# Kernel tuning notes

Hardware: AMD Instinct MI355X
Metric: run time of the kernel (lower is better)

## Reference

```python
import jax, jax.numpy as jnp
import numpy as np

B, S, H = 16, 4096, 512   # batch, seq frames, conv_dim[-1]
G, V, D = 2, 320, 256     # groups, codevectors per group, codevector_dim


def setup_inputs() -> dict:
    key = jax.random.key(0)
    k1, k2, k3 = jax.random.split(key, 3)
    hidden_states = jax.random.normal(k1, (B, S, H), dtype=jnp.float32)
    W = jax.random.normal(k2, (H, G * V), dtype=jnp.float32) * 0.02
    b = jnp.zeros((G * V,), dtype=jnp.float32)
    codevectors = jax.random.normal(k3, (1, G * V, D // G), dtype=jnp.float32)
    return {"hidden_states": hidden_states, "W": W, "b": b,
            "codevectors": codevectors, "num_groups": G}


def reference(hidden_states, W, b, codevectors, num_groups):
    Bb, Ss, Hh = hidden_states.shape
    GV = W.shape[1]
    g = num_groups
    v = GV // g
    d = codevectors.shape[-1]
    BT = Bb * Ss

    # weight_proj: [B,S,H] @ [H, G*V] -> logits per (token, group, var)
    logits = (hidden_states @ W + b).reshape(BT, g, v)

    # eval path: hard argmax one-hot over codevectors per group
    idx = jnp.argmax(logits, axis=-1)              # [BT, g] int

    # one-hot x codebook multiply-reduce == gather from codebook
    cb = codevectors.reshape(g, v, d)              # [g, v, d]
    gathered = cb[jnp.arange(g)[None, :], idx]     # [BT, g, d]
    out = gathered.reshape(Bb, Ss, g * d)          # [B, S, codevector_dim]

    # perplexity over one-hot probs: marginal = mean of one-hots = counts/BT
    marginal = jnp.zeros((g, v), dtype=jnp.float32)
    marginal = marginal.at[jnp.arange(g)[None, :], idx].add(1.0) / BT
    perplexity = jnp.exp(-jnp.sum(marginal * jnp.log(marginal + 1e-7), axis=-1)).sum()

    return out, perplexity
```

## Files before the change

kernel.cpp:

```cpp
#include <hip/hip_runtime.h>
#include <hip/hip_bf16.h>
#include <hip/hip_fp8.h>

constexpr int BT = 65536;
constexpr int K  = 512;
constexpr int V  = 320;
constexpr int G  = 2;
constexpr int Dg = 128;
constexpr int MT = 64;
constexpr int NSTEP = 8;
constexpr size_t WS_IMG = 4096;

using f32x4 = __attribute__((ext_vector_type(4))) float;

static __device__ __forceinline__ unsigned cvt4(float a, float b, float c, float d) {
#if __has_builtin(__builtin_amdgcn_cvt_pk_fp8_f32)
    int r = 0;
    r = __builtin_amdgcn_cvt_pk_fp8_f32(a, b, r, false);
    r = __builtin_amdgcn_cvt_pk_fp8_f32(c, d, r, true);
    return (unsigned)r;
#else
    __hip_fp8_e4m3 ha(a), hb(b), hc(c), hd(d);
    return (unsigned)ha.__x | ((unsigned)hb.__x << 8) |
           ((unsigned)hc.__x << 16) | ((unsigned)hd.__x << 24);
#endif
}
static __device__ __forceinline__ long long mk64(unsigned lo, unsigned hi) {
    return (long long)(((unsigned long long)hi << 32) | lo);
}
static __device__ __forceinline__ f32x4 mfma_fp8(long long a, long long b, f32x4 c) {
    return __builtin_amdgcn_mfma_f32_16x16x32_fp8_fp8(a, b, c, 0, 0, 0);
}

__global__ __launch_bounds__(256) void vq_prep(const float* __restrict__ Wm,
                                               unsigned char* __restrict__ img)
{
    int id   = blockIdx.x * 256 + threadIdx.x;
    int lane = id & 63;
    int r    = id >> 6;
    int nt   = r % 5;  r /= 5;
    int wc   = r & 3;  r >>= 2;
    int s    = r & 7;
    int g    = r >> 3;
    int col  = g * V + wc * 80 + nt * 16 + (lane & 15);
    int kb   = s * 64 + (lane >> 4) * 8;
    float v0[8], v1[8];
#pragma unroll
    for (int j = 0; j < 8; ++j) {
        v0[j] = 16.0f * Wm[(size_t)(kb + j) * 640 + col];
        v1[j] = 16.0f * Wm[(size_t)(kb + 32 + j) * 640 + col];
    }
    *reinterpret_cast<uint4*>(img + (size_t)id * 16) =
        make_uint4(cvt4(v0[0], v0[1], v0[2], v0[3]), cvt4(v0[4], v0[5], v0[6], v0[7]),
                   cvt4(v1[0], v1[1], v1[2], v1[3]), cvt4(v1[4], v1[5], v1[6], v1[7]));
}

__global__ __launch_bounds__(512) void vq_main(
    const float* __restrict__ hs, const unsigned char* __restrict__ img,
    const float* __restrict__ bv, const float* __restrict__ cbv,
    float* __restrict__ out, unsigned int* __restrict__ hist)
{
    __shared__ __align__(16) unsigned char smem[8192];

    const int tid  = threadIdx.x;
    const int bid  = blockIdx.x;
    const int g    = (bid >> 3) & 1;
    const int rblk = (bid & 7) | ((bid >> 4) << 3);
    const int r0   = rblk * MT;
    const int w    = tid >> 6;
    const int lane = tid & 63;
    const int l4   = lane & 15;
    const int wc   = w & 3;
    const int h    = w >> 2;

    f32x4 acc[2][5] = {};

    const int arow = tid >> 3, akq = tid & 7;
    const float* aptr = hs + (size_t)(r0 + arow) * K + akq * 8;
    const int awoff = (arow >> 4) * 1024 + ((arow & 15) + 16 * (akq & 3)) * 16 + (akq >> 2) * 8;
    const int a_rd0 = (h * 2 + 0) * 1024 + lane * 16;
    const int a_rd1 = (h * 2 + 1) * 1024 + lane * 16;
    const unsigned char* bwv = img + (size_t)g * 163840 + wc * 5120 + (size_t)lane * 16;

    auto packA = [&](float4 x, float4 y, int sel) {
        *reinterpret_cast<uint2*>(&smem[sel * 4096 + awoff]) =
            make_uint2(cvt4(x.x, x.y, x.z, x.w), cvt4(y.x, y.y, y.z, y.w));
    };

    float4 aX[2], aY[2];
    aX[0] = *reinterpret_cast<const float4*>(aptr);
    aY[0] = *reinterpret_cast<const float4*>(aptr + 4);
    packA(aX[0], aY[0], 0);
    aX[1] = *reinterpret_cast<const float4*>(aptr + 64);
    aY[1] = *reinterpret_cast<const float4*>(aptr + 64 + 4);
    __syncthreads();

#pragma unroll
    for (int s = 0; s < NSTEP; ++s) {
        const int cur = s & 1, nxt = cur ^ 1;
        if (s + 1 < NSTEP) packA(aX[nxt], aY[nxt], nxt);
        if (s + 2 < NSTEP) {
            aX[cur] = *reinterpret_cast<const float4*>(aptr + (s + 2) * 64);
            aY[cur] = *reinterpret_cast<const float4*>(aptr + (s + 2) * 64 + 4);
        }
        const unsigned char* bs = bwv + (size_t)s * 20480;
        __builtin_amdgcn_s_setprio(1);
        {
            uint4 b0 = *reinterpret_cast<const uint4*>(bs);
            uint4 b1 = *reinterpret_cast<const uint4*>(bs + 1024);
            uint4 b2 = *reinterpret_cast<const uint4*>(bs + 2048);
            uint4 b3 = *reinterpret_cast<const uint4*>(bs + 3072);
            uint4 b4 = *reinterpret_cast<const uint4*>(bs + 4096);
            uint4 a0 = *reinterpret_cast<const uint4*>(&smem[cur * 4096 + a_rd0]);
            uint4 a1 = *reinterpret_cast<const uint4*>(&smem[cur * 4096 + a_rd1]);
            long long a0k0 = mk64(a0.x, a0.y), a0k1 = mk64(a0.z, a0.w);
            long long a1k0 = mk64(a1.x, a1.y), a1k1 = mk64(a1.z, a1.w);
            uint4 bb[5] = {b0, b1, b2, b3, b4};
#pragma unroll
            for (int nt = 0; nt < 5; ++nt) {
                long long bk0 = mk64(bb[nt].x, bb[nt].y), bk1 = mk64(bb[nt].z, bb[nt].w);
                acc[0][nt] = mfma_fp8(a0k0, bk0, acc[0][nt]);
                acc[0][nt] = mfma_fp8(a0k1, bk1, acc[0][nt]);
                acc[1][nt] = mfma_fp8(a1k0, bk0, acc[1][nt]);
                acc[1][nt] = mfma_fp8(a1k1, bk1, acc[1][nt]);
            }
        }
        __builtin_amdgcn_s_setprio(0);
        __syncthreads();
    }

    float biasv[5];
#pragma unroll
    for (int nt = 0; nt < 5; ++nt) biasv[nt] = 16.0f * bv[g * V + wc * 80 + nt * 16 + l4];

    float* red_v = reinterpret_cast<float*>(smem);
    int*   red_i = reinterpret_cast<int*>(smem + 1024);
    int*   idx_s = reinterpret_cast<int*>(smem + 2048);

#pragma unroll
    for (int mt = 0; mt < 2; ++mt) {
#pragma unroll
        for (int reg = 0; reg < 4; ++reg) {
            float bestv = acc[mt][0][reg] + biasv[0];
            int   besti = wc * 80 + l4;
#pragma unroll
            for (int nt = 1; nt < 5; ++nt) {
                float v = acc[mt][nt][reg] + biasv[nt];
                int   ci = wc * 80 + nt * 16 + l4;
                if (v > bestv) { bestv = v; besti = ci; }
            }
#pragma unroll
            for (int m = 1; m < 16; m <<= 1) {
                float ov = __shfl_xor(bestv, m);
                int   oi = __shfl_xor(besti, m);
                if (ov > bestv || (ov == bestv && oi < besti)) { bestv = ov; besti = oi; }
            }
            if (l4 == 0) {
                int row = h * 32 + mt * 16 + (lane >> 4) * 4 + reg;
                red_v[row * 4 + wc] = bestv;
                red_i[row * 4 + wc] = besti;
            }
        }
    }
    __syncthreads();

    int my_bi = -1;
    if (tid < MT) {
        float bb = red_v[tid * 4]; int bi = red_i[tid * 4];
#pragma unroll
        for (int c = 1; c < 4; ++c) {
            float v = red_v[tid * 4 + c]; int ii = red_i[tid * 4 + c];
            if (v > bb || (v == bb && ii < bi)) { bb = v; bi = ii; }
        }
        idx_s[tid] = bi;
        my_bi = bi;
    }
    __syncthreads();

#pragma unroll
    for (int i = 0; i < 4; ++i) {
        int idx = i * 512 + tid;
        int row = idx >> 5;
        int d4  = idx & 31;
        int vi  = idx_s[row];
        float4 val = *reinterpret_cast<const float4*>(&cbv[((size_t)(g * V + vi)) * Dg + d4 * 4]);
        *reinterpret_cast<float4*>(&out[((size_t)(r0 + row)) * (G * Dg) + g * Dg + d4 * 4]) = val;
    }
    if (my_bi >= 0) atomicAdd(&hist[g * V + my_bi], 1u);
}

__global__ void vq_ppl(const unsigned int* __restrict__ hist, float* __restrict__ outp)
{
    int lane = threadIdx.x;
    float ppl = 0.0f;
    for (int g = 0; g < G; ++g) {
        float local = 0.0f;
        for (int v = lane; v < V; v += 64) {
            float m = (float)hist[g * V + v] * (1.0f / (float)BT);
            local += m * logf(m + 1e-7f);
        }
#pragma unroll
        for (int off = 32; off; off >>= 1) local += __shfl_down(local, off);
        if (lane == 0) ppl += expf(-local);
    }
    if (lane == 0) outp[0] = ppl;
}

extern "C" void kernel_launch(void* const* d_in, const int* in_sizes, int n_in,
                              void* d_out, int out_size, void* d_ws, size_t ws_size,
                              hipStream_t stream)
{
    const float* hs  = (const float*)d_in[0];
    const float* Wm  = (const float*)d_in[1];
    const float* bv  = (const float*)d_in[2];
    const float* cbv = (const float*)d_in[3];
    float* out = (float*)d_out;

    unsigned int*  hist = (unsigned int*)d_ws;
    unsigned char* img  = (unsigned char*)d_ws + WS_IMG;

    hipMemsetAsync(d_ws, 0, G * V * sizeof(unsigned int), stream);
    vq_prep<<<80, 256, 0, stream>>>(Wm, img);
    vq_main<<<2048, 512, 0, stream>>>(hs, img, bv, cbv, out, hist);
    vq_ppl<<<1, 64, 0, stream>>>(hist, out + (size_t)BT * G * Dg);
}
```

Measured before the change: 88.60 us.

## Process both groups per block, staging full fp8 A tile in LDS once

New measurement: 98.87 us. 1.12x slower.

```diff
diff --git a/kernel.cpp b/kernel.cpp
--- a/kernel.cpp
+++ b/kernel.cpp
@@ -60,62 +60,56 @@
     const float* __restrict__ bv, const float* __restrict__ cbv,
     float* __restrict__ out, unsigned int* __restrict__ hist)
 {
-    __shared__ __align__(16) unsigned char smem[8192];
+    __shared__ __align__(16) unsigned char smem[35072];
 
     const int tid  = threadIdx.x;
     const int bid  = blockIdx.x;
-    const int g    = (bid >> 3) & 1;
-    const int rblk = (bid & 7) | ((bid >> 4) << 3);
-    const int r0   = rblk * MT;
+    const int r0   = bid * MT;
     const int w    = tid >> 6;
     const int lane = tid & 63;
     const int l4   = lane & 15;
     const int wc   = w & 3;
     const int h    = w >> 2;
 
-    f32x4 acc[2][5] = {};
-
-    const int arow = tid >> 3, akq = tid & 7;
-    const float* aptr = hs + (size_t)(r0 + arow) * K + akq * 8;
-    const int awoff = (arow >> 4) * 1024 + ((arow & 15) + 16 * (akq & 3)) * 16 + (akq >> 2) * 8;
+    {
+        const int arow = tid >> 3, akq = tid & 7;
+        const float* aptr = hs + (size_t)(r0 + arow) * K + akq * 8;
+        const int awoff = (arow >> 4) * 1024 + ((arow & 15) + 16 * (akq & 3)) * 16 + (akq >> 2) * 8;
+#pragma unroll
+        for (int s = 0; s < NSTEP; ++s) {
+            float4 x = *reinterpret_cast<const float4*>(aptr + s * 64);
+            float4 y = *reinterpret_cast<const float4*>(aptr + s * 64 + 4);
+            *reinterpret_cast<uint2*>(&smem[s * 4096 + awoff]) =
+                make_uint2(cvt4(x.x, x.y, x.z, x.w), cvt4(y.x, y.y, y.z, y.w));
+        }
+    }
+    __syncthreads();
+
     const int a_rd0 = (h * 2 + 0) * 1024 + lane * 16;
     const int a_rd1 = (h * 2 + 1) * 1024 + lane * 16;
-    const unsigned char* bwv = img + (size_t)g * 163840 + wc * 5120 + (size_t)lane * 16;
-
-    auto packA = [&](float4 x, float4 y, int sel) {
-        *reinterpret_cast<uint2*>(&smem[sel * 4096 + awoff]) =
-            make_uint2(cvt4(x.x, x.y, x.z, x.w), cvt4(y.x, y.y, y.z, y.w));
-    };
-
-    float4 aX[2], aY[2];
-    aX[0] = *reinterpret_cast<const float4*>(aptr);
-    aY[0] = *reinterpret_cast<const float4*>(aptr + 4);
-    packA(aX[0], aY[0], 0);
-    aX[1] = *reinterpret_cast<const float4*>(aptr + 64);
-    aY[1] = *reinterpret_cast<const float4*>(aptr + 64 + 4);
-    __syncthreads();
-
-#pragma unroll
-    for (int s = 0; s < NSTEP; ++s) {
-        const int cur = s & 1, nxt = cur ^ 1;
-        if (s + 1 < NSTEP) packA(aX[nxt], aY[nxt], nxt);
-        if (s + 2 < NSTEP) {
-            aX[cur] = *reinterpret_cast<const float4*>(aptr + (s + 2) * 64);
-            aY[cur] = *reinterpret_cast<const float4*>(aptr + (s + 2) * 64 + 4);
-        }
-        const unsigned char* bs = bwv + (size_t)s * 20480;
-        __builtin_amdgcn_s_setprio(1);
-        {
+
+    float* red_v = reinterpret_cast<float*>(smem + 32768);
+    int*   red_i = reinterpret_cast<int*>(smem + 33792);
+    int*   idx_s = reinterpret_cast<int*>(smem + 34816);
+
+    for (int g = 0; g < G; ++g) {
+        f32x4 acc[2][5] = {};
+        const unsigned char* bg = img + (size_t)g * 163840 + wc * 5120 + (size_t)lane * 16;
+
+#pragma unroll
+        for (int s = 0; s < NSTEP; ++s) {
+            const unsigned char* bs = bg + (size_t)s * 20480;
             uint4 b0 = *reinterpret_cast<const uint4*>(bs);
             uint4 b1 = *reinterpret_cast<const uint4*>(bs + 1024);
             uint4 b2 = *reinterpret_cast<const uint4*>(bs + 2048);
             uint4 b3 = *reinterpret_cast<const uint4*>(bs + 3072);
             uint4 b4 = *reinterpret_cast<const uint4*>(bs + 4096);
-            uint4 a0 = *reinterpret_cast<const uint4*>(&smem[cur * 4096 + a_rd0]);
-            uint4 a1 = *reinterpret_cast<const uint4*>(&smem[cur * 4096 + a_rd1]);
+            uint4 a0 = *reinterpret_cast<const uint4*>(&smem[s * 4096 + a_rd0]);
+            uint4 a1 = *reinterpret_cast<const uint4*>(&smem[s * 4096 + a_rd1]);
             long long a0k0 = mk64(a0.x, a0.y), a0k1 = mk64(a0.z, a0.w);
             long long a1k0 = mk64(a1.x, a1.y), a1k1 = mk64(a1.z, a1.w);
             uint4 bb[5] = {b0, b1, b2, b3, b4};
+            __builtin_amdgcn_s_setprio(1);
 #pragma unroll
             for (int nt = 0; nt < 5; ++nt) {
                 long long bk0 = mk64(bb[nt].x, bb[nt].y), bk1 = mk64(bb[nt].z, bb[nt].w);
@@ -124,69 +118,63 @@
                 acc[1][nt] = mfma_fp8(a1k0, bk0, acc[1][nt]);
                 acc[1][nt] = mfma_fp8(a1k1, bk1, acc[1][nt]);
             }
-        }
-        __builtin_amdgcn_s_setprio(0);
+            __builtin_amdgcn_s_setprio(0);
+        }
+
         __syncthreads();
-    }
-
-    float biasv[5];
-#pragma unroll
-    for (int nt = 0; nt < 5; ++nt) biasv[nt] = 16.0f * bv[g * V + wc * 80 + nt * 16 + l4];
-
-    float* red_v = reinterpret_cast<float*>(smem);
-    int*   red_i = reinterpret_cast<int*>(smem + 1024);
-    int*   idx_s = reinterpret_cast<int*>(smem + 2048);
-
-#pragma unroll
-    for (int mt = 0; mt < 2; ++mt) {
-#pragma unroll
-        for (int reg = 0; reg < 4; ++reg) {
-            float bestv = acc[mt][0][reg] + biasv[0];
-            int   besti = wc * 80 + l4;
-#pragma unroll
-            for (int nt = 1; nt < 5; ++nt) {
-                float v = acc[mt][nt][reg] + biasv[nt];
-                int   ci = wc * 80 + nt * 16 + l4;
-                if (v > bestv) { bestv = v; besti = ci; }
+        float biasv[5];
+#pragma unroll
+        for (int nt = 0; nt < 5; ++nt) biasv[nt] = 16.0f * bv[g * V + wc * 80 + nt * 16 + l4];
+
+#pragma unroll
+        for (int mt = 0; mt < 2; ++mt) {
+#pragma unroll
+            for (int reg = 0; reg < 4; ++reg) {
+                float bestv = acc[mt][0][reg] + biasv[0];
+                int   besti = wc * 80 + l4;
+#pragma unroll
+                for (int nt = 1; nt < 5; ++nt) {
+                    float v = acc[mt][nt][reg] + biasv[nt];
+                    int   ci = wc * 80 + nt * 16 + l4;
+                    if (v > bestv) { bestv = v; besti = ci; }
+                }
+#pragma unroll
+                for (int m = 1; m < 16; m <<= 1) {
+                    float ov = __shfl_xor(bestv, m);
+                    int   oi = __shfl_xor(besti, m);
+                    if (ov > bestv || (ov == bestv && oi < besti)) { bestv = ov; besti = oi; }
+                }
+                if (l4 == 0) {
+                    int row = h * 32 + mt * 16 + (lane >> 4) * 4 + reg;
+                    red_v[row * 4 + wc] = bestv;
+                    red_i[row * 4 + wc] = besti;
+                }
             }
-#pragma unroll
-            for (int m = 1; m < 16; m <<= 1) {
-                float ov = __shfl_xor(bestv, m);
-                int   oi = __shfl_xor(besti, m);
-                if (ov > bestv || (ov == bestv && oi < besti)) { bestv = ov; besti = oi; }
+        }
+        __syncthreads();
+
+        if (tid < MT) {
+            float bb = red_v[tid * 4]; int bi = red_i[tid * 4];
+#pragma unroll
+            for (int c = 1; c < 4; ++c) {
+                float v = red_v[tid * 4 + c]; int ii = red_i[tid * 4 + c];
+                if (v > bb || (v == bb && ii < bi)) { bb = v; bi = ii; }
             }
-            if (l4 == 0) {
-                int row = h * 32 + mt * 16 + (lane >> 4) * 4 + reg;
-                red_v[row * 4 + wc] = bestv;
-                red_i[row * 4 + wc] = besti;
-            }
-        }
-    }
-    __syncthreads();
-
-    int my_bi = -1;
-    if (tid < MT) {
-        float bb = red_v[tid * 4]; int bi = red_i[tid * 4];
-#pragma unroll
-        for (int c = 1; c < 4; ++c) {
-            float v = red_v[tid * 4 + c]; int ii = red_i[tid * 4 + c];
-            if (v > bb || (v == bb && ii < bi)) { bb = v; bi = ii; }
-        }
-        idx_s[tid] = bi;
-        my_bi = bi;
-    }
-    __syncthreads();
-
-#pragma unroll
-    for (int i = 0; i < 4; ++i) {
-        int idx = i * 512 + tid;
-        int row = idx >> 5;
-        int d4  = idx & 31;
-        int vi  = idx_s[row];
-        float4 val = *reinterpret_cast<const float4*>(&cbv[((size_t)(g * V + vi)) * Dg + d4 * 4]);
-        *reinterpret_cast<float4*>(&out[((size_t)(r0 + row)) * (G * Dg) + g * Dg + d4 * 4]) = val;
-    }
-    if (my_bi >= 0) atomicAdd(&hist[g * V + my_bi], 1u);
+            idx_s[tid] = bi;
+            atomicAdd(&hist[g * V + bi], 1u);
+        }
+        __syncthreads();
+
+#pragma unroll
+        for (int i = 0; i < 4; ++i) {
+            int idx = i * 512 + tid;
+            int row = idx >> 5;
+            int d4  = idx & 31;
+            int vi  = idx_s[row];
+            float4 val = *reinterpret_cast<const float4*>(&cbv[((size_t)(g * V + vi)) * Dg + d4 * 4]);
+            *reinterpret_cast<float4*>(&out[((size_t)(r0 + row)) * (G * Dg) + g * Dg + d4 * 4]) = val;
+        }
+    }
 }
 
 __global__ void vq_ppl(const unsigned int* __restrict__ hist, float* __restrict__ outp)
@@ -221,6 +209,6 @@
 
     hipMemsetAsync(d_ws, 0, G * V * sizeof(unsigned int), stream);
     vq_prep<<<80, 256, 0, stream>>>(Wm, img);
-    vq_main<<<2048, 512, 0, stream>>>(hs, img, bv, cbv, out, hist);
+    vq_main<<<1024, 512, 0, stream>>>(hs, img, bv, cbv, out, hist);
     vq_ppl<<<1, 64, 0, stream>>>(hist, out + (size_t)BT * G * Dg);
 }
```

## Stage weight tiles into LDS via async global_load_lds double buffering

Applied to the files above, without the earlier changes.

After: 90.64 us. +2.3%, slower.

```diff
diff --git a/kernel.cpp b/kernel.cpp
--- a/kernel.cpp
+++ b/kernel.cpp
@@ -60,7 +60,7 @@
     const float* __restrict__ bv, const float* __restrict__ cbv,
     float* __restrict__ out, unsigned int* __restrict__ hist)
 {
-    __shared__ __align__(16) unsigned char smem[8192];
+    __shared__ __align__(16) unsigned char smem[49152];
 
     const int tid  = threadIdx.x;
     const int bid  = blockIdx.x;
@@ -80,45 +80,59 @@
     const int awoff = (arow >> 4) * 1024 + ((arow & 15) + 16 * (akq & 3)) * 16 + (akq >> 2) * 8;
     const int a_rd0 = (h * 2 + 0) * 1024 + lane * 16;
     const int a_rd1 = (h * 2 + 1) * 1024 + lane * 16;
-    const unsigned char* bwv = img + (size_t)g * 163840 + wc * 5120 + (size_t)lane * 16;
-
-    auto packA = [&](float4 x, float4 y, int sel) {
-        *reinterpret_cast<uint2*>(&smem[sel * 4096 + awoff]) =
+    const unsigned char* bsrc = img + (size_t)g * 163840 + (size_t)tid * 16;
+    const int b_rd = 8192 + wc * 5 * 1024 + lane * 16;
+
+    auto issueB = [&](int s, int buf) {
+        const unsigned char* bs = bsrc + (size_t)s * 20480;
+        const int dst = 8192 + buf * 20480;
+#pragma unroll
+        for (int i = 0; i < 2; ++i)
+            __builtin_amdgcn_global_load_lds(
+                (const __attribute__((address_space(1))) void*)(bs + i * 8192),
+                (__attribute__((address_space(3))) void*)(&smem[dst + i * 8192 + tid * 16]),
+                16, 0, 0);
+        if (tid < 256)
+            __builtin_amdgcn_global_load_lds(
+                (const __attribute__((address_space(1))) void*)(bs + 16384),
+                (__attribute__((address_space(3))) void*)(&smem[dst + 16384 + tid * 16]),
+                16, 0, 0);
+    };
+    auto packA = [&](float4 x, float4 y, int buf) {
+        *reinterpret_cast<uint2*>(&smem[buf * 4096 + awoff]) =
             make_uint2(cvt4(x.x, x.y, x.z, x.w), cvt4(y.x, y.y, y.z, y.w));
     };
 
     float4 aX[2], aY[2];
     aX[0] = *reinterpret_cast<const float4*>(aptr);
     aY[0] = *reinterpret_cast<const float4*>(aptr + 4);
-    packA(aX[0], aY[0], 0);
+    issueB(0, 0);
     aX[1] = *reinterpret_cast<const float4*>(aptr + 64);
     aY[1] = *reinterpret_cast<const float4*>(aptr + 64 + 4);
+    packA(aX[0], aY[0], 0);
     __syncthreads();
 
 #pragma unroll
     for (int s = 0; s < NSTEP; ++s) {
         const int cur = s & 1, nxt = cur ^ 1;
-        if (s + 1 < NSTEP) packA(aX[nxt], aY[nxt], nxt);
+        if (s + 1 < NSTEP) issueB(s + 1, nxt);
         if (s + 2 < NSTEP) {
             aX[cur] = *reinterpret_cast<const float4*>(aptr + (s + 2) * 64);
             aY[cur] = *reinterpret_cast<const float4*>(aptr + (s + 2) * 64 + 4);
         }
-        const unsigned char* bs = bwv + (size_t)s * 20480;
+        __builtin_amdgcn_sched_barrier(0);
+        if (s + 1 < NSTEP) packA(aX[nxt], aY[nxt], nxt);
         __builtin_amdgcn_s_setprio(1);
         {
-            uint4 b0 = *reinterpret_cast<const uint4*>(bs);
-            uint4 b1 = *reinterpret_cast<const uint4*>(bs + 1024);
-            uint4 b2 = *reinterpret_cast<const uint4*>(bs + 2048);
-            uint4 b3 = *reinterpret_cast<const uint4*>(bs + 3072);
-            uint4 b4 = *reinterpret_cast<const uint4*>(bs + 4096);
             uint4 a0 = *reinterpret_cast<const uint4*>(&smem[cur * 4096 + a_rd0]);
             uint4 a1 = *reinterpret_cast<const uint4*>(&smem[cur * 4096 + a_rd1]);
             long long a0k0 = mk64(a0.x, a0.y), a0k1 = mk64(a0.z, a0.w);
             long long a1k0 = mk64(a1.x, a1.y), a1k1 = mk64(a1.z, a1.w);
-            uint4 bb[5] = {b0, b1, b2, b3, b4};
 #pragma unroll
             for (int nt = 0; nt < 5; ++nt) {
-                long long bk0 = mk64(bb[nt].x, bb[nt].y), bk1 = mk64(bb[nt].z, bb[nt].w);
+                uint4 bb = *reinterpret_cast<const uint4*>(
+                    &smem[b_rd + cur * 20480 + nt * 1024]);
+                long long bk0 = mk64(bb.x, bb.y), bk1 = mk64(bb.z, bb.w);
                 acc[0][nt] = mfma_fp8(a0k0, bk0, acc[0][nt]);
                 acc[0][nt] = mfma_fp8(a0k1, bk1, acc[0][nt]);
                 acc[1][nt] = mfma_fp8(a1k0, bk0, acc[1][nt]);
```
